# Kernel tuning notes

Hardware: AMD Instinct MI355X
Metric: run time of the kernel (lower is better)

## Reference

```python
import jax, jax.numpy as jnp
import numpy as np

N = 256          # num_nodes per graph
B = 64           # batch_size (len(data.y))
NLAY = 3
F_IN = 5
NE = N * N       # num_edges per graph
NN = B * N       # total nodes
TEMP = 0.6
ALPHA = 0.1      # propagation residual alpha
BB_ALPHA = 0.8   # BBEdge_pred alpha
K = 2


def setup_inputs() -> dict:
    key = jax.random.key(0)
    ks = jax.random.split(key, 8)
    n_tril = N * (N + 1) // 2
    x = jax.random.normal(ks[0], (NN, F_IN), jnp.float32)
    # lower-triangular (incl. diagonal) entries of the learned adjacency
    edge_weight_param = jax.random.normal(ks[1], (n_tril,), jnp.float32)
    # BBEdge_pred params per layer (torch init: U(1.0,1.5), U(0.49,0.51))
    a_uc = 1.0 + 0.5 * jax.random.uniform(ks[2], (NLAY,), jnp.float32)
    b_uc = 0.49 + 0.02 * jax.random.uniform(ks[3], (NLAY,), jnp.float32)
    # randomness for Kumaraswamy pi sample and RelaxedBernoulli rsample
    u_pi = jax.random.uniform(ks[4], (NLAY,), jnp.float32)
    u_rb = jax.random.uniform(ks[5], (NLAY, NE), jnp.float32)
    lin_w = jax.random.normal(ks[6], (F_IN, 128), jnp.float32) / np.float32(np.sqrt(F_IN))
    lin_b = jnp.zeros((128,), jnp.float32)
    fc_w = jax.random.normal(ks[7], (128, 3), jnp.float32) / np.float32(np.sqrt(128))
    fc_b = jnp.zeros((3,), jnp.float32)
    # dense block-diagonal edge_index: graph b owns nodes [b*N, (b+1)*N); edge k=i*N+j -> (i,j)
    base = jnp.arange(N, dtype=jnp.int32)
    rows = jnp.repeat(base, N)
    cols = jnp.tile(base, N)
    offs = (jnp.arange(B, dtype=jnp.int32) * N)[:, None]
    edge_index = jnp.stack([(offs + rows[None, :]).reshape(-1),
                            (offs + cols[None, :]).reshape(-1)])
    batch = jnp.repeat(jnp.arange(B, dtype=jnp.int32), N)
    return {"x": x, "edge_weight_param": edge_weight_param, "a_uc": a_uc, "b_uc": b_uc,
            "u_pi": u_pi, "u_rb": u_rb, "lin_w": lin_w, "lin_b": lin_b,
            "fc_w": fc_w, "fc_b": fc_b, "edge_index": edge_index, "batch": batch}


def _forward(x, edge_weight_param, a_uc, b_uc, u_pi, u_rb,
             lin_w, lin_b, fc_w, fc_b, edge_index, batch):
    row, col = edge_index[0], edge_index[1]
    # symmetrized dense edge-weight matrix from tril params
    xs, ys = jnp.tril_indices(N)
    W = jnp.zeros((N, N), x.dtype).at[xs, ys].set(edge_weight_param)
    W = W + W.T - jnp.diag(jnp.diag(W))
    w_full = jnp.tile(W.reshape(-1), B)                      # [E]
    # GCN-style degree normalization (self-loops already on diagonal)
    deg = jax.ops.segment_sum(jnp.abs(w_full), row, num_segments=NN)
    dis = jnp.where(deg > 0, deg ** -0.5, 0.0)
    adj = dis[row] * w_full * dis[col]                       # [E]

    # Beta-Bernoulli edge keep-prob and RelaxedBernoulli masks
    a = jax.nn.softplus(jnp.clip(a_uc, -10.0, None))
    b = jax.nn.softplus(jnp.clip(b_uc, -10.0, 50.0))
    up = jnp.clip(u_pi, 1e-6, 1.0 - 1e-6)
    pi = (1.0 - up ** (1.0 / b)) ** (1.0 / a)                # [NLAY]
    ur = jnp.clip(u_rb, 1e-6, 1.0 - 1e-6)
    logits = jnp.log(pi) - jnp.log1p(-pi)                    # [NLAY]
    z = jax.nn.sigmoid((logits[:, None] + jnp.log(ur) - jnp.log1p(-ur)) / TEMP)  # [NLAY, NE]

    def conv(xx, w_e):
        # emb = alpha*x + (1-alpha)/K * scatter(col, w_e * x[row])
        msg = w_e[:, None] * xx[row]                          # [E, F]
        agg = jax.ops.segment_sum(msg, col, num_segments=NN)
        return ALPHA * xx + (1.0 - ALPHA) / K * agg

    emb = ALPHA * x
    # layer 0: masked adjacency
    x1 = conv(x, jnp.tile(z[0], B) * adj)
    emb = emb + (1.0 - ALPHA) * x1 / NLAY
    # layer 1 (middle): unmasked conv, then masked block conv (nblock=1, fp=5)
    x2 = conv(x1, adj)
    emb = emb + (1.0 - ALPHA) * x2 / NLAY
    x3 = jax.nn.relu(conv(x2[:, :F_IN], jnp.tile(z[1], B) * adj))  # dropout off (eval)
    # layer 2 (last)
    x4 = conv(x3, adj)
    emb = emb + (1.0 - ALPHA) * x4 / NLAY
    o = conv(x4, jnp.tile(z[2], B) * adj)
    out = jax.nn.relu(o @ lin_w + lin_b)                      # [NN, 128]

    # KL regularizer summed over layers
    euler = 0.577215664901532
    kld = ((1.0 - BB_ALPHA / a) * (-euler - jax.scipy.special.digamma(b) - 1.0 / b)
           + jnp.log(a * b + 1e-10) - jnp.log(jnp.float32(BB_ALPHA)) - (b - 1.0) / b)
    kld_loss = jnp.sum(kld)

    pooled = jax.ops.segment_sum(out, batch, num_segments=B)  # global_add_pool -> [B, 128]
    output = pooled @ fc_w + fc_b                             # [B, 3]
    drop_rates = pi[:, None]                                  # [NLAY, 1]
    return output, kld_loss, drop_rates


def reference(x, edge_weight_param, a_uc, b_uc, u_pi, u_rb,
              lin_w, lin_b, fc_w, fc_b, edge_index, batch):
    return _forward(x, edge_weight_param, a_uc, b_uc, u_pi, u_rb,
                    lin_w, lin_b, fc_w, fc_b, edge_index, batch)
```

## Files before the change

### kernel.cpp

```cpp
#include <hip/hip_runtime.h>
#include <math.h>

#define NN_ 256
#define BB_ 64
#define FF_ 5
#define NE_ 65536

#define OFF_SLA 0
#define OFF_SL1 65536
#define OFF_SL3 131072
#define OFF_SL5 196608
#define OFF_DIS 262144
#define OFF_LG  262400

__global__ __launch_bounds__(256) void k_dis(
    const float* __restrict__ p, const float* __restrict__ a_uc,
    const float* __restrict__ b_uc, const float* __restrict__ u_pi,
    float* __restrict__ ws, float* __restrict__ out) {
  const int i = blockIdx.x, k = threadIdx.x;
  const int t = (i >= k) ? (i * (i + 1) / 2 + k) : (k * (k + 1) / 2 + i);
  __shared__ float sh[NN_];
  sh[k] = fabsf(p[t]);
  __syncthreads();
  for (int s = NN_ / 2; s > 0; s >>= 1) {
    if (k < s) sh[k] += sh[k + s];
    __syncthreads();
  }
  if (k == 0) {
    const float deg = sh[0];
    ws[OFF_DIS + i] = (deg > 0.0f) ? (1.0f / sqrtf(deg)) : 0.0f;
  }

  if (i == 0 && k == 0) {
    float kld_sum = 0.0f;
    const float euler = 0.577215664901532f;
    for (int l = 0; l < 3; ++l) {
      const float au = fmaxf(a_uc[l], -10.0f);
      const float bu = fminf(fmaxf(b_uc[l], -10.0f), 50.0f);
      const float a = log1pf(expf(au));
      const float b = log1pf(expf(bu));
      const float up = fminf(fmaxf(u_pi[l], 1e-6f), 1.0f - 1e-6f);
      const float pi = powf(1.0f - powf(up, 1.0f / b), 1.0f / a);
      ws[OFF_LG + l] = logf(pi) - log1pf(-pi);
      out[193 + l] = pi;
      float x = b, dg = 0.0f;
      while (x < 6.0f) { dg -= 1.0f / x; x += 1.0f; }
      const float inv = 1.0f / x, inv2 = inv * inv;
      dg += logf(x) - 0.5f * inv
            - inv2 * (1.0f / 12.0f - inv2 * (1.0f / 120.0f - inv2 * (1.0f / 252.0f)));
      kld_sum += (1.0f - 0.8f / a) * (-euler - dg - 1.0f / b)
                 + logf(a * b + 1e-10f) - logf(0.8f) - (b - 1.0f) / b;
    }
    out[192] = kld_sum;
  }
}

__global__ __launch_bounds__(256) void build_ops(
    const float* __restrict__ p, const float* __restrict__ u_rb,
    float* __restrict__ ws) {
  const int i = blockIdx.x, j = threadIdx.x;
  const float disi = ws[OFF_DIS + i];
  const float disj = ws[OFF_DIS + j];
  const float lg0 = ws[OFF_LG + 0];
  const float lg1 = ws[OFF_LG + 1];
  const float lg2 = ws[OFF_LG + 2];

  const int t = (i >= j) ? (i * (i + 1) / 2 + j) : (j * (j + 1) / 2 + i);
  const float w = p[t];
  const float adj = disi * w * disj;
  const float dlt = (i == j) ? 0.1f : 0.0f;
  const int idx = i * NN_ + j;
  const float inv_temp = 1.0f / 0.6f;

  ws[OFF_SLA + idx] = 0.45f * adj + dlt;

  float u, v, z;
  u = fminf(fmaxf(u_rb[0 * NE_ + idx], 1e-6f), 1.0f - 1e-6f);
  v = (lg0 + logf(u) - log1pf(-u)) * inv_temp;
  z = 1.0f / (1.0f + expf(-v));
  ws[OFF_SL1 + idx] = 0.45f * z * adj + dlt;

  u = fminf(fmaxf(u_rb[1 * NE_ + idx], 1e-6f), 1.0f - 1e-6f);
  v = (lg1 + logf(u) - log1pf(-u)) * inv_temp;
  z = 1.0f / (1.0f + expf(-v));
  ws[OFF_SL3 + idx] = 0.45f * z * adj + dlt;

  u = fminf(fmaxf(u_rb[2 * NE_ + idx], 1e-6f), 1.0f - 1e-6f);
  v = (lg2 + logf(u) - log1pf(-u)) * inv_temp;
  z = 1.0f / (1.0f + expf(-v));
  ws[OFF_SL5 + idx] = 0.45f * z * adj + dlt;
}

__global__ __launch_bounds__(1024) void batch_chain(
    const float* __restrict__ x0g, const float* __restrict__ ws,
    const float* __restrict__ lin_w, const float* __restrict__ lin_b,
    const float* __restrict__ fc_w, const float* __restrict__ fc_b,
    float* __restrict__ out) {
  const int b = blockIdx.x, tid = threadIdx.x;
  __shared__ float xbuf[2][NN_ * 8];
  __shared__ float part[4 * NN_ * 8];
  float* Xc = xbuf[0];
  float* Xn = xbuf[1];

  for (int idx = tid; idx < NN_ * FF_; idx += 1024) {
    const int i = idx / 5, f = idx - 5 * i;
    Xc[i * 8 + f] = x0g[b * (NN_ * FF_) + idx];
  }
  __syncthreads();

  const int q = tid >> 8;
  const int j = tid & 255;
  const int k0 = q * 64;

#pragma unroll
  for (int l = 0; l < 5; ++l) {
    const float* __restrict__ Op =
        ws + (l == 0 ? OFF_SL1 : l == 2 ? OFF_SL3 : l == 4 ? OFF_SL5 : OFF_SLA)
        + j;
    float4 a03 = {0.f, 0.f, 0.f, 0.f};
    float a4 = 0.f;
#pragma unroll 8
    for (int k = k0; k < k0 + 64; ++k) {
      const float w = Op[k * NN_];
      const float4 xv = *(const float4*)(Xc + k * 8);
      const float x4 = Xc[k * 8 + 4];
      a03.x += w * xv.x; a03.y += w * xv.y;
      a03.z += w * xv.z; a03.w += w * xv.w;
      a4 += w * x4;
    }
    *(float4*)(part + tid * 8) = a03;
    part[tid * 8 + 4] = a4;
    __syncthreads();
    for (int idx = tid; idx < 2048; idx += 1024) {
      const float sum = part[idx] + part[2048 + idx] + part[4096 + idx] +
                        part[6144 + idx];
      float y = 0.1f * Xc[idx] + 0.45f * sum;
      if (l == 2) y = fmaxf(y, 0.f);
      Xn[idx] = y;
    }
    __syncthreads();
    float* t = Xc; Xc = Xn; Xn = t;
  }

  const int k = tid & 127, seg = tid >> 7;
  const float lw0 = lin_w[0 * 128 + k];
  const float lw1 = lin_w[1 * 128 + k];
  const float lw2 = lin_w[2 * 128 + k];
  const float lw3 = lin_w[3 * 128 + k];
  const float lw4 = lin_w[4 * 128 + k];
  const float lb = lin_b[k];
  float acc = 0.f;
  const int j0 = seg * 32;
#pragma unroll 4
  for (int jj = j0; jj < j0 + 32; ++jj) {
    const float4 ov = *(const float4*)(Xc + jj * 8);
    const float o4 = Xc[jj * 8 + 4];
    const float v = lb + lw0 * ov.x + lw1 * ov.y + lw2 * ov.z +
                    lw3 * ov.w + lw4 * o4;
    acc += fmaxf(v, 0.f);
  }
  part[seg * 128 + k] = acc;
  __syncthreads();
  if (tid < 128) {
    float s = 0.f;
#pragma unroll
    for (int s8 = 0; s8 < 8; ++s8) s += part[s8 * 128 + tid];
    part[tid] = s;
  }
  __syncthreads();
  if (tid < 3) {
    float s = fc_b[tid];
    for (int kk = 0; kk < 128; ++kk) s += part[kk] * fc_w[kk * 3 + tid];
    out[b * 3 + tid] = s;
  }
}

extern "C" void kernel_launch(void* const* d_in, const int* in_sizes, int n_in,
                              void* d_out, int out_size, void* d_ws,
                              size_t ws_size, hipStream_t stream) {
  const float* x      = (const float*)d_in[0];
  const float* p      = (const float*)d_in[1];
  const float* a_uc   = (const float*)d_in[2];
  const float* b_uc   = (const float*)d_in[3];
  const float* u_pi   = (const float*)d_in[4];
  const float* u_rb   = (const float*)d_in[5];
  const float* lin_w  = (const float*)d_in[6];
  const float* lin_b  = (const float*)d_in[7];
  const float* fc_w   = (const float*)d_in[8];
  const float* fc_b   = (const float*)d_in[9];
  float* out = (float*)d_out;
  float* ws  = (float*)d_ws;

  k_dis<<<256, 256, 0, stream>>>(p, a_uc, b_uc, u_pi, ws, out);
  build_ops<<<256, 256, 0, stream>>>(p, u_rb, ws);
  batch_chain<<<64, 1024, 0, stream>>>(x, ws, lin_w, lin_b, fc_w, fc_b, out);
}
```

Before: 133.9 us.

## Fuse degree and operator kernels by factoring symmetric normalization into chain

Merges the degree/KL kernel and the operator-building kernel into one launch. The D^-1/2 normalization is no longer baked into the stored operators: each row of X is prescaled by dis before the matmul and the output is scaled by dis afterward. This lets the operators be written without waiting for the row-sum reduction. The cost is two extra shared-memory buffers and extra scaling work in batch_chain. The identity-plus-0.1 diagonal term also appears to be dropped from the stored operator and handled through the 0.1*X residual instead.

```diff
diff --git a/kernel.cpp b/kernel.cpp
--- a/kernel.cpp
+++ b/kernel.cpp
@@ -11,84 +11,74 @@
 #define OFF_SL3 131072
 #define OFF_SL5 196608
 #define OFF_DIS 262144
-#define OFF_LG  262400
 
-__global__ __launch_bounds__(256) void k_dis(
-    const float* __restrict__ p, const float* __restrict__ a_uc,
-    const float* __restrict__ b_uc, const float* __restrict__ u_pi,
-    float* __restrict__ ws, float* __restrict__ out) {
-  const int i = blockIdx.x, k = threadIdx.x;
-  const int t = (i >= k) ? (i * (i + 1) / 2 + k) : (k * (k + 1) / 2 + i);
+__global__ __launch_bounds__(256) void build_all(
+    const float* __restrict__ p, const float* __restrict__ u_rb,
+    const float* __restrict__ a_uc, const float* __restrict__ b_uc,
+    const float* __restrict__ u_pi, float* __restrict__ ws,
+    float* __restrict__ out) {
+  const int i = blockIdx.x, j = threadIdx.x;
+  const int t = (i >= j) ? (i * (i + 1) / 2 + j) : (j * (j + 1) / 2 + i);
+  const float w = p[t];
+
   __shared__ float sh[NN_];
-  sh[k] = fabsf(p[t]);
-  __syncthreads();
-  for (int s = NN_ / 2; s > 0; s >>= 1) {
-    if (k < s) sh[k] += sh[k + s];
-    __syncthreads();
-  }
-  if (k == 0) {
-    const float deg = sh[0];
-    ws[OFF_DIS + i] = (deg > 0.0f) ? (1.0f / sqrtf(deg)) : 0.0f;
-  }
+  __shared__ float slg[3];
+  __shared__ float skld[3];
+  sh[j] = fabsf(w);
 
-  if (i == 0 && k == 0) {
-    float kld_sum = 0.0f;
-    const float euler = 0.577215664901532f;
-    for (int l = 0; l < 3; ++l) {
-      const float au = fmaxf(a_uc[l], -10.0f);
-      const float bu = fminf(fmaxf(b_uc[l], -10.0f), 50.0f);
-      const float a = log1pf(expf(au));
-      const float b = log1pf(expf(bu));
-      const float up = fminf(fmaxf(u_pi[l], 1e-6f), 1.0f - 1e-6f);
-      const float pi = powf(1.0f - powf(up, 1.0f / b), 1.0f / a);
-      ws[OFF_LG + l] = logf(pi) - log1pf(-pi);
+  if (j < 3) {
+    const int l = j;
+    const float au = fmaxf(a_uc[l], -10.0f);
+    const float bu = fminf(fmaxf(b_uc[l], -10.0f), 50.0f);
+    const float a = log1pf(expf(au));
+    const float b = log1pf(expf(bu));
+    const float up = fminf(fmaxf(u_pi[l], 1e-6f), 1.0f - 1e-6f);
+    const float pi = powf(1.0f - powf(up, 1.0f / b), 1.0f / a);
+    slg[l] = logf(pi) - log1pf(-pi);
+    if (i == 0) {
       out[193 + l] = pi;
       float x = b, dg = 0.0f;
       while (x < 6.0f) { dg -= 1.0f / x; x += 1.0f; }
       const float inv = 1.0f / x, inv2 = inv * inv;
       dg += logf(x) - 0.5f * inv
             - inv2 * (1.0f / 12.0f - inv2 * (1.0f / 120.0f - inv2 * (1.0f / 252.0f)));
-      kld_sum += (1.0f - 0.8f / a) * (-euler - dg - 1.0f / b)
-                 + logf(a * b + 1e-10f) - logf(0.8f) - (b - 1.0f) / b;
+      const float euler = 0.577215664901532f;
+      skld[l] = (1.0f - 0.8f / a) * (-euler - dg - 1.0f / b)
+                + logf(a * b + 1e-10f) - logf(0.8f) - (b - 1.0f) / b;
     }
-    out[192] = kld_sum;
   }
-}
+  __syncthreads();
 
-__global__ __launch_bounds__(256) void build_ops(
-    const float* __restrict__ p, const float* __restrict__ u_rb,
-    float* __restrict__ ws) {
-  const int i = blockIdx.x, j = threadIdx.x;
-  const float disi = ws[OFF_DIS + i];
-  const float disj = ws[OFF_DIS + j];
-  const float lg0 = ws[OFF_LG + 0];
-  const float lg1 = ws[OFF_LG + 1];
-  const float lg2 = ws[OFF_LG + 2];
+  for (int s = NN_ / 2; s > 0; s >>= 1) {
+    if (j < s) sh[j] += sh[j + s];
+    __syncthreads();
+  }
+  if (j == 0) {
+    const float deg = sh[0];
+    ws[OFF_DIS + i] = (deg > 0.0f) ? (1.0f / sqrtf(deg)) : 0.0f;
+    if (i == 0) out[192] = skld[0] + skld[1] + skld[2];
+  }
 
-  const int t = (i >= j) ? (i * (i + 1) / 2 + j) : (j * (j + 1) / 2 + i);
-  const float w = p[t];
-  const float adj = disi * w * disj;
-  const float dlt = (i == j) ? 0.1f : 0.0f;
+  const float lg0 = slg[0];
+  const float lg1 = slg[1];
+  const float lg2 = slg[2];
   const int idx = i * NN_ + j;
   const float inv_temp = 1.0f / 0.6f;
 
-  ws[OFF_SLA + idx] = 0.45f * adj + dlt;
+  ws[OFF_SLA + idx] = w;
 
-  float u, v, z;
+  float u, v;
   u = fminf(fmaxf(u_rb[0 * NE_ + idx], 1e-6f), 1.0f - 1e-6f);
   v = (lg0 + logf(u) - log1pf(-u)) * inv_temp;
-  z = 1.0f / (1.0f + expf(-v));
-  ws[OFF_SL1 + idx] = 0.45f * z * adj + dlt;
+  ws[OFF_SL1 + idx] = w / (1.0f + expf(-v));
 
   u = fminf(fmaxf(u_rb[1 * NE_ + idx], 1e-6f), 1.0f - 1e-6f);
   v = (lg1 + logf(u) - log1pf(-u)) * inv_temp;
-  z = 1.0f / (1.0f + expf(-v));
-  ws[OFF_SL3 + idx] = 0.45f * z * adj + dlt;
+  ws[OFF_SL3 + idx] = w / (1.0f + expf(-v));
 
   u = fminf(fmaxf(u_rb[2 * NE_ + idx], 1e-6f), 1.0f - 1e-6f);
   v = (lg2 + logf(u) - log1pf(-u)) * inv_temp;
-  z = 1.0f / (1.0f + expf(-v));
-  ws[OFF_SL5 + idx] = 0.45f * z * adj + dlt;
+  ws[OFF_SL5 + idx] = w / (1.0f + expf(-v));
 }
 
 __global__ __launch_bounds__(1024) void batch_chain(
@@ -98,14 +88,22 @@
     float* __restrict__ out) {
   const int b = blockIdx.x, tid = threadIdx.x;
   __shared__ float xbuf[2][NN_ * 8];
+  __shared__ float sbuf[2][NN_ * 8];
   __shared__ float part[4 * NN_ * 8];
+  __shared__ float sdis[NN_];
   float* Xc = xbuf[0];
   float* Xn = xbuf[1];
+  float* Sc = sbuf[0];
+  float* Sn = sbuf[1];
 
+  for (int ii = tid; ii < NN_; ii += 1024) sdis[ii] = ws[OFF_DIS + ii];
   for (int idx = tid; idx < NN_ * FF_; idx += 1024) {
     const int i = idx / 5, f = idx - 5 * i;
     Xc[i * 8 + f] = x0g[b * (NN_ * FF_) + idx];
   }
+  __syncthreads();
+  for (int idx = tid; idx < 2048; idx += 1024)
+    Sc[idx] = sdis[idx >> 3] * Xc[idx];
   __syncthreads();
 
   const int q = tid >> 8;
@@ -121,12 +119,12 @@
     float a4 = 0.f;
 #pragma unroll 8
     for (int k = k0; k < k0 + 64; ++k) {
-      const float w = Op[k * NN_];
-      const float4 xv = *(const float4*)(Xc + k * 8);
-      const float x4 = Xc[k * 8 + 4];
-      a03.x += w * xv.x; a03.y += w * xv.y;
-      a03.z += w * xv.z; a03.w += w * xv.w;
-      a4 += w * x4;
+      const float wv = Op[k * NN_];
+      const float4 xv = *(const float4*)(Sc + k * 8);
+      const float x4 = Sc[k * 8 + 4];
+      a03.x += wv * xv.x; a03.y += wv * xv.y;
+      a03.z += wv * xv.z; a03.w += wv * xv.w;
+      a4 += wv * x4;
     }
     *(float4*)(part + tid * 8) = a03;
     part[tid * 8 + 4] = a4;
@@ -134,12 +132,15 @@
     for (int idx = tid; idx < 2048; idx += 1024) {
       const float sum = part[idx] + part[2048 + idx] + part[4096 + idx] +
                         part[6144 + idx];
-      float y = 0.1f * Xc[idx] + 0.45f * sum;
+      const float dj = sdis[idx >> 3];
+      float y = 0.1f * Xc[idx] + 0.45f * dj * sum;
       if (l == 2) y = fmaxf(y, 0.f);
       Xn[idx] = y;
+      Sn[idx] = dj * y;
     }
     __syncthreads();
-    float* t = Xc; Xc = Xn; Xn = t;
+    float* tp = Xc; Xc = Xn; Xn = tp;
+    tp = Sc; Sc = Sn; Sn = tp;
   }
 
   const int k = tid & 127, seg = tid >> 7;
@@ -155,9 +156,9 @@
   for (int jj = j0; jj < j0 + 32; ++jj) {
     const float4 ov = *(const float4*)(Xc + jj * 8);
     const float o4 = Xc[jj * 8 + 4];
-    const float v = lb + lw0 * ov.x + lw1 * ov.y + lw2 * ov.z +
-                    lw3 * ov.w + lw4 * o4;
-    acc += fmaxf(v, 0.f);
+    const float vv = lb + lw0 * ov.x + lw1 * ov.y + lw2 * ov.z +
+                     lw3 * ov.w + lw4 * o4;
+    acc += fmaxf(vv, 0.f);
   }
   part[seg * 128 + k] = acc;
   __syncthreads();
@@ -191,7 +192,6 @@
   float* out = (float*)d_out;
   float* ws  = (float*)d_ws;
 
-  k_dis<<<256, 256, 0, stream>>>(p, a_uc, b_uc, u_pi, ws, out);
-  build_ops<<<256, 256, 0, stream>>>(p, u_rb, ws);
+  build_all<<<256, 256, 0, stream>>>(p, u_rb, a_uc, b_uc, u_pi, ws, out);
   batch_chain<<<64, 1024, 0, stream>>>(x, ws, lin_w, lin_b, fc_w, fc_b, out);
 }
```

Measured after the change: 128.0 us. -4.5%, faster.
